# Optimization experiments

Hardware: AMD Instinct MI355X
Metric: run time of the kernel (lower is better)

The kernel has to match this reference:

```python
import jax, jax.numpy as jnp
import numpy as np

B, S, D_IN, D_OUT = 4, 4096, 256, 256

def setup_inputs() -> dict:
    key = jax.random.key(0)
    ks = jax.random.split(key, 7)
    scale = 1.0 / np.sqrt(D_IN)
    return {
        "x": jax.random.normal(ks[0], (B, S, D_IN), dtype=jnp.float32),
        "Wq": jax.random.uniform(ks[1], (D_IN, D_OUT), jnp.float32, -scale, scale),
        "bq": jax.random.uniform(ks[2], (D_OUT,), jnp.float32, -scale, scale),
        "Wk": jax.random.uniform(ks[3], (D_IN, D_OUT), jnp.float32, -scale, scale),
        "bk": jax.random.uniform(ks[4], (D_OUT,), jnp.float32, -scale, scale),
        "Wv": jax.random.uniform(ks[5], (D_IN, D_OUT), jnp.float32, -scale, scale),
        "bv": jax.random.uniform(ks[6], (D_OUT,), jnp.float32, -scale, scale),
    }

def reference(x, Wq, bq, Wk, bk, Wv, bv):
    # QKV projections: [B, S, D_OUT]
    q = jnp.einsum("bsd,de->bse", x, Wq) + bq
    k = jnp.einsum("bsd,de->bse", x, Wk) + bk
    v = jnp.einsum("bsd,de->bse", x, Wv) + bv
    # Scaled dot-product attention; full [B, S, S] scores as in the original.
    scores = jnp.einsum("bqe,bke->bqk", q, k) / jnp.sqrt(jnp.asarray(q.shape[-1], q.dtype))
    attn = jax.nn.softmax(scores, axis=-1)
    return jnp.einsum("bqk,bke->bqe", attn, v)
```

## Files before the change

kernel.cpp:

```cpp
#include <hip/hip_runtime.h>
#include <stdint.h>

typedef unsigned short u16;
typedef long long i64;
typedef __attribute__((ext_vector_type(4))) float f32x4;
typedef __attribute__((ext_vector_type(8))) short bf16x8;
typedef __attribute__((ext_vector_type(4))) int i32x4;
typedef __attribute__((ext_vector_type(2))) unsigned int u32x2;

#define SEQ 4096
#define DIM 256
#define QS4 0.36067376f

__device__ __forceinline__ u16 f2bf(float f) {
  union { float f; uint32_t u; } v; v.f = f;
  uint32_t r = (v.u + 0x7FFFu + ((v.u >> 16) & 1u)) >> 16;
  return (u16)r;
}

__device__ __forceinline__ uint8_t f2fp8(float f) {
  return (uint8_t)__builtin_amdgcn_cvt_pk_fp8_f32(f, 0.f, 0, false);
}

__device__ __forceinline__ void gload_lds16(const void* g, void* lds) {
  __builtin_amdgcn_global_load_lds(
      (const __attribute__((address_space(1))) uint32_t*)g,
      (__attribute__((address_space(3))) uint32_t*)lds, 16, 0, 0);
}

__device__ __forceinline__ f32x4 mfma8(i64 a, i64 b, f32x4 c) {
  return __builtin_amdgcn_mfma_f32_16x16x32_fp8_fp8(a, b, c, 0, 0, 0);
}

__global__ __launch_bounds__(256) void wt_kernel(const float* __restrict__ Wq,
                                                 const float* __restrict__ Wk,
                                                 const float* __restrict__ Wv,
                                                 u16* __restrict__ wt) {
  int b = blockIdx.x;
  int w = b >> 8;
  int n = b & 255;
  const float* W = (w == 0) ? Wq : ((w == 1) ? Wk : Wv);
  float scale = (w == 0) ? QS4 : ((w == 1) ? 0.25f : 1.0f);
  int k = threadIdx.x;
  wt[(w * 256 + n) * 256 + k] = f2bf(W[k * 256 + n] * scale);
}

__global__ __launch_bounds__(256) void qkv_kernel(
    const float* __restrict__ x, const float* __restrict__ bq,
    const float* __restrict__ bk, const float* __restrict__ bv,
    const u16* __restrict__ wt, uint8_t* __restrict__ qs,
    uint8_t* __restrict__ kk, char* __restrict__ vt) {
  __shared__ __align__(16) char lds_b[65536];
  __shared__ __align__(16) u16 lds_v[4096];
  int tid = threadIdx.x;
  int w = tid >> 6, l = tid & 63;
  int a = l & 15, g = l >> 4;
  int rowbase = blockIdx.x * 64;

  uint32_t wso[8];
#pragma unroll
  for (int j = 0; j < 8; ++j) {
    uint32_t inst = w * 8 + j;
    uint32_t flat = inst * 1024 + l * 16;
    uint32_t row = flat >> 9;
    uint32_t c5 = (flat >> 4) & 31;
    uint32_t sc = (c5 & ~7u) | ((c5 ^ row) & 7u);
    wso[j] = row * 512 + sc * 16;
  }
  uint32_t bro[8];
#pragma unroll
  for (int ks = 0; ks < 8; ++ks) {
    uint32_t c5 = ks * 4 + g;
    uint32_t sc = (c5 & ~7u) | ((c5 ^ (a & 7u)) & 7u);
    bro[ks] = (uint32_t)a * 512 + sc * 16;
  }

  bf16x8 afr[8];
  {
    int row = rowbase + w * 16 + a;
    const f32x4* xr4 = (const f32x4*)(x + (size_t)row * 256);
#pragma unroll
    for (int ks = 0; ks < 8; ++ks) {
      int q4 = ks * 8 + g * 2;
      f32x4 lo = xr4[q4], hi = xr4[q4 + 1];
      union { bf16x8 s; u16 u[8]; } fr;
      fr.u[0] = f2bf(lo[0]); fr.u[1] = f2bf(lo[1]);
      fr.u[2] = f2bf(lo[2]); fr.u[3] = f2bf(lo[3]);
      fr.u[4] = f2bf(hi[0]); fr.u[5] = f2bf(hi[1]);
      fr.u[6] = f2bf(hi[2]); fr.u[7] = f2bf(hi[3]);
      afr[ks] = fr.s;
    }
  }

#pragma unroll
  for (int j = 0; j < 8; ++j)
    gload_lds16((const char*)wt + wso[j], lds_b + (w * 8 + j) * 1024);

  int cur = 0;
  for (int it = 0; it < 12; ++it) {
    asm volatile("s_waitcnt vmcnt(0) lgkmcnt(0)" ::: "memory");
    __builtin_amdgcn_s_barrier();
    __builtin_amdgcn_sched_barrier(0);
    if (it < 11) {
#pragma unroll
      for (int j = 0; j < 8; ++j)
        gload_lds16((const char*)wt + (size_t)(it + 1) * 32768 + wso[j],
                    lds_b + (cur ^ 1) * 32768 + (w * 8 + j) * 1024);
    }
    int w3 = it >> 2, qn = it & 3;
    f32x4 acc[4];
#pragma unroll
    for (int n0 = 0; n0 < 4; ++n0) acc[n0] = (f32x4){0.f, 0.f, 0.f, 0.f};
#pragma unroll
    for (int ks = 0; ks < 8; ++ks) {
#pragma unroll
      for (int n0 = 0; n0 < 4; ++n0) {
        bf16x8 bfr = *(const bf16x8*)(lds_b + cur * 32768 + bro[ks] + n0 * 8192);
        acc[n0] = __builtin_amdgcn_mfma_f32_16x16x32_bf16(afr[ks], bfr, acc[n0], 0, 0, 0);
      }
    }
    const float* bias = (w3 == 0) ? bq : ((w3 == 1) ? bk : bv);
    if (w3 < 2) {
      uint8_t* out8 = (w3 == 0) ? qs : kk;
      float bscale = (w3 == 0) ? QS4 : 0.25f;
#pragma unroll
      for (int n0 = 0; n0 < 4; ++n0) {
        int col = qn * 64 + n0 * 16 + a;
        float bb = bias[col] * bscale;
#pragma unroll
        for (int r = 0; r < 4; ++r) {
          int row = rowbase + w * 16 + g * 4 + r;
          out8[(size_t)row * 256 + col] = f2fp8(acc[n0][r] + bb);
        }
      }
    } else {
#pragma unroll
      for (int n0 = 0; n0 < 4; ++n0) {
        int col = qn * 64 + n0 * 16 + a;
        float bb = bias[col];
        int dl = n0 * 16 + a;
#pragma unroll
        for (int r = 0; r < 4; ++r) {
          int m = w * 16 + g * 4 + r;
          uint32_t byteoff =
              (uint32_t)dl * 128 + ((((uint32_t)m >> 3) ^ ((uint32_t)dl & 7)) << 4) + (m & 7) * 2;
          *(u16*)((char*)lds_v + byteoff) = f2bf(acc[n0][r] + bb);
        }
      }
      asm volatile("s_waitcnt lgkmcnt(0)" ::: "memory");
      __builtin_amdgcn_s_barrier();
      {
        int dl = tid >> 2;
        size_t base = (size_t)blockIdx.x * 32768 + (size_t)(qn * 64 + dl) * 128;
#pragma unroll
        for (int cc = 0; cc < 2; ++cc) {
          uint32_t c = (tid & 3) + cc * 4;
          i32x4 vd = *(const i32x4*)((const char*)lds_v + dl * 128 + ((c ^ (dl & 7)) << 4));
          *(i32x4*)(vt + base + c * 16) = vd;
        }
      }
    }
    cur ^= 1;
  }
}

#define VVB 32768u
#define PVB 98304u

#define PV_STEP(SLOT)                                                          \
  {                                                                            \
    bf16x8 pfr[2][2];                                                          \
    _Pragma("unroll") for (int mt = 0; mt < 2; ++mt)                           \
    _Pragma("unroll") for (int j2 = 0; j2 < 2; ++j2)                           \
        pfr[mt][j2] = *(const bf16x8*)(lds + PVB + (SLOT) * 16384 + pro[j2] +  \
                                       mt * 2048);                             \
    __builtin_amdgcn_s_setprio(1);                                             \
    _Pragma("unroll") for (int mt = 0; mt < 2; ++mt)                           \
    _Pragma("unroll") for (int j2 = 0; j2 < 2; ++j2)                           \
        lacc[mt] = __builtin_amdgcn_mfma_f32_16x16x32_bf16(pfr[mt][j2], ones,  \
                                                           lacc[mt], 0, 0, 0); \
    _Pragma("unroll") for (int d0 = 0; d0 < 8; ++d0)                           \
    _Pragma("unroll") for (int j2 = 0; j2 < 2; ++j2) {                         \
      bf16x8 vfr = *(const bf16x8*)(lds + VVB + (SLOT) * 32768 + vro[j2] +     \
                                    d0 * 2048);                                \
      o[0][d0] = __builtin_amdgcn_mfma_f32_16x16x32_bf16(pfr[0][j2], vfr, o[0][d0], 0, 0, 0); \
      o[1][d0] = __builtin_amdgcn_mfma_f32_16x16x32_bf16(pfr[1][j2], vfr, o[1][d0], 0, 0, 0); \
    }                                                                          \
    __builtin_amdgcn_s_setprio(0);                                             \
  }

#define TILE(CUR, DO_PV, DO_K)                                                 \
  {                                                                            \
    asm volatile("s_waitcnt vmcnt(0) lgkmcnt(0)" ::: "memory");                \
    __builtin_amdgcn_s_barrier();                                              \
    __builtin_amdgcn_sched_barrier(0);                                         \
    _Pragma("unroll") for (int j = 0; j < 4; ++j)                              \
        gload_lds16(vstp + vso[j], lds + VVB + (CUR) * 32768 + (w * 4 + j) * 1024); \
    if (DO_K) {                                                                \
      gload_lds16(kstp + kso[0], lds + ((CUR) ^ 1) * 16384 + (w * 2 + 0) * 1024); \
      gload_lds16(kstp + kso[1], lds + ((CUR) ^ 1) * 16384 + (w * 2 + 1) * 1024); \
    }                                                                          \
    kstp += 16384;                                                             \
    vstp += 32768;                                                             \
    f32x4 sc[2][2];                                                            \
    _Pragma("unroll") for (int mt = 0; mt < 2; ++mt)                           \
    _Pragma("unroll") for (int n = 0; n < 2; ++n)                              \
        sc[mt][n] = (f32x4){0.f, 0.f, 0.f, 0.f};                               \
    __builtin_amdgcn_s_setprio(1);                                             \
    _Pragma("unroll") for (int n = 0; n < 2; ++n)                              \
    _Pragma("unroll") for (int j = 0; j < 8; ++j) {                            \
      i64 kfr = *(const i64*)(lds + (CUR) * 16384 + kro[j] + n * 4096);        \
      sc[0][n] = mfma8(kfr, qfr[0][j], sc[0][n]);                              \
      sc[1][n] = mfma8(kfr, qfr[1][j], sc[1][n]);                              \
    }                                                                          \
    __builtin_amdgcn_s_setprio(0);                                             \
    _Pragma("unroll") for (int mt = 0; mt < 2; ++mt)                           \
    _Pragma("unroll") for (int n = 0; n < 2; ++n) {                            \
      float e0 = exp2f(sc[mt][n][0]);                                          \
      float e1 = exp2f(sc[mt][n][1]);                                          \
      float e2 = exp2f(sc[mt][n][2]);                                          \
      float e3 = exp2f(sc[mt][n][3]);                                          \
      uint32_t p0 = (uint32_t)f2bf(e0) | ((uint32_t)f2bf(e1) << 16);           \
      uint32_t p1 = (uint32_t)f2bf(e2) | ((uint32_t)f2bf(e3) << 16);           \
      u32x2 pk = {p0, p1};                                                     \
      *(u32x2*)(lds + PVB + (CUR) * 16384 + pwo[n] + mt * 2048) = pk;          \
    }                                                                          \
    if (DO_PV) PV_STEP((CUR) ^ 1)                                              \
  }

__global__ __launch_bounds__(512, 1) void attn_kernel(
    const uint8_t* __restrict__ qs, const uint8_t* __restrict__ kk,
    const char* __restrict__ vt, float* __restrict__ out,
    float* __restrict__ pOB, float* __restrict__ pl, int split) {
  __shared__ __align__(16) char lds[131072];
  int tid = threadIdx.x;
  int w = tid >> 6, l = tid & 63;
  int a = l & 15, g = l >> 4;
  int qq = w >> 1, sub = w & 1;
  int bx = blockIdx.x;
  int h, batch, qt;
  if (split == 2) { h = bx & 1; batch = (bx >> 1) & 3; qt = bx >> 3; }
  else            { h = 0;      batch = (bx >> 1) & 3; qt = ((bx >> 3) << 1) | (bx & 1); }
  int ntHalf = (split == 2) ? 16 : 32;

  uint32_t a7 = a & 7;
  uint32_t kro[8], vro[2], pro[2], pwo[2], kso[2], vso[4];
  {
    uint32_t row = (uint32_t)(sub * 32 + a);
#pragma unroll
    for (int j = 0; j < 8; ++j) {
      uint32_t c4 = j * 2 + (g >> 1);
      kro[j] = row * 256 + (((c4 & ~7u) | ((c4 ^ a7) & 7u)) << 4) + (g & 1) * 8;
    }
  }
#pragma unroll
  for (int j2 = 0; j2 < 2; ++j2)
    vro[j2] = (uint32_t)(sub * 128 + a) * 128 +
              ((((uint32_t)(j2 * 4 + g)) ^ a7) << 4);
  {
    uint32_t q = (uint32_t)(qq * 32 + a);
#pragma unroll
    for (int j2 = 0; j2 < 2; ++j2)
      pro[j2] = q * 128 + ((((uint32_t)(j2 * 4 + g)) ^ a7) << 4);
#pragma unroll
    for (int n = 0; n < 2; ++n)
      pwo[n] = q * 128 +
               ((((uint32_t)(sub * 4 + n * 2 + (g >> 1))) ^ a7) << 4) + (g & 1) * 8;
  }
#pragma unroll
  for (int j = 0; j < 2; ++j) {
    uint32_t inst = w * 2 + j, flat = inst * 1024 + l * 16;
    uint32_t row = flat >> 8, c4 = (flat >> 4) & 15;
    kso[j] = row * 256 + (((c4 & ~7u) | ((c4 ^ (row & 7u)) & 7u)) << 4);
  }
#pragma unroll
  for (int j = 0; j < 4; ++j) {
    uint32_t inst = w * 4 + j, flat = inst * 1024 + l * 16;
    uint32_t row = flat >> 7, c3 = (flat >> 4) & 7;
    vso[j] = row * 128 + ((c3 ^ (row & 7)) << 4);
  }

  i64 qfr[2][8];
  {
    const uint8_t* qp = qs + (size_t)(batch * SEQ + qt * 128) * 256;
#pragma unroll
    for (int mt = 0; mt < 2; ++mt)
#pragma unroll
      for (int j = 0; j < 8; ++j)
        qfr[mt][j] = *(const i64*)(qp + (size_t)(qq * 32 + mt * 16 + a) * 256 +
                                   j * 32 + g * 8);
  }

  f32x4 o[2][8];
  f32x4 lacc[2];
#pragma unroll
  for (int mt = 0; mt < 2; ++mt) {
    lacc[mt] = (f32x4){0.f, 0.f, 0.f, 0.f};
#pragma unroll
    for (int d0 = 0; d0 < 8; ++d0) o[mt][d0] = (f32x4){0.f, 0.f, 0.f, 0.f};
  }
  const short ob = (short)0x3F80;
  bf16x8 ones = {ob, ob, ob, ob, ob, ob, ob, ob};

  const uint8_t* kstp = kk + (size_t)batch * SEQ * 256 + (size_t)h * 2048 * 256;
  const char* vstp = vt + (size_t)batch * 64 * 32768 + (size_t)h * 32 * 32768;

  gload_lds16(kstp + kso[0], lds + (w * 2 + 0) * 1024);
  gload_lds16(kstp + kso[1], lds + (w * 2 + 1) * 1024);
  kstp += 16384;

  TILE(0, false, true)
  for (int tp = 0; tp < ntHalf - 1; ++tp) {
    TILE(1, true, true)
    TILE(0, true, true)
  }
  TILE(1, true, false)

  asm volatile("s_waitcnt vmcnt(0) lgkmcnt(0)" ::: "memory");
  __builtin_amdgcn_s_barrier();
  __builtin_amdgcn_sched_barrier(0);
  PV_STEP(1)

  float* po = (h == 0) ? out : pOB;
  size_t obase = (size_t)(batch * SEQ + qt * 128 + qq * 32) * 256 + sub * 128;
#pragma unroll
  for (int mt = 0; mt < 2; ++mt)
#pragma unroll
    for (int r = 0; r < 4; ++r) {
#pragma unroll
      for (int d0 = 0; d0 < 8; ++d0)
        po[obase + (size_t)(mt * 16 + g * 4 + r) * 256 + d0 * 16 + a] = o[mt][d0][r];
    }
  if (a == 0 && sub == 0) {
#pragma unroll
    for (int mt = 0; mt < 2; ++mt)
#pragma unroll
      for (int r = 0; r < 4; ++r)
        pl[h * 16384 + (batch * 32 + qt) * 128 + qq * 32 + mt * 16 + g * 4 + r] =
            lacc[mt][r];
  }
}

__global__ __launch_bounds__(256) void combine_kernel(float* __restrict__ out,
                                                      const float* __restrict__ pOB,
                                                      const float* __restrict__ pl,
                                                      int split) {
  int b = blockIdx.x;
  int tid = threadIdx.x;
  int batch = b >> 12;
  int rem = b & 4095;
  int qt = rem >> 7, ql = rem & 127;
  size_t idx = (size_t)b * 256 + tid;
  int li = (batch * 32 + qt) * 128 + ql;
  float lA = pl[li];
  float v;
  if (split == 2) {
    float lB = pl[16384 + li];
    v = (out[idx] + pOB[idx]) / (lA + lB);
  } else {
    v = out[idx] / lA;
  }
  out[idx] = v;
}

extern "C" void kernel_launch(void* const* d_in, const int* in_sizes, int n_in,
                              void* d_out, int out_size, void* d_ws, size_t ws_size,
                              hipStream_t stream) {
  const float* x = (const float*)d_in[0];
  const float* Wq = (const float*)d_in[1];
  const float* bq = (const float*)d_in[2];
  const float* Wk = (const float*)d_in[3];
  const float* bk = (const float*)d_in[4];
  const float* Wv = (const float*)d_in[5];
  const float* bv = (const float*)d_in[6];
  char* ws = (char*)d_ws;
  u16* wt = (u16*)ws;
  uint8_t* qs = (uint8_t*)(ws + 0x60000);
  uint8_t* kk = (uint8_t*)(ws + 0x460000);
  char* vt = ws + 0x860000;
  float* pl = (float*)(ws + 0x1060000);
  float* pOB = (float*)(ws + 0x1080000);
  int split = (ws_size >= 0x2080000ull) ? 2 : 1;
  wt_kernel<<<dim3(768), dim3(256), 0, stream>>>(Wq, Wk, Wv, wt);
  qkv_kernel<<<dim3(256), dim3(256), 0, stream>>>(x, bq, bk, bv, wt, qs, kk, vt);
  attn_kernel<<<dim3(split * 128), dim3(512), 0, stream>>>(qs, kk, vt, (float*)d_out,
                                                           pOB, pl, split);
  combine_kernel<<<dim3(16384), dim3(256), 0, stream>>>((float*)d_out, pOB, pl, split);
}
```

Measured before the change: 118.3 us.

## Stagger QK/PV order across odd/even waves and store split partial output in bf16

New measurement: 120.8 us. +2.1%, slower.

```diff
diff --git a/kernel.cpp b/kernel.cpp
--- a/kernel.cpp
+++ b/kernel.cpp
@@ -16,6 +16,11 @@
   union { float f; uint32_t u; } v; v.f = f;
   uint32_t r = (v.u + 0x7FFFu + ((v.u >> 16) & 1u)) >> 16;
   return (u16)r;
+}
+
+__device__ __forceinline__ float bf2f(u16 u) {
+  union { uint32_t u; float f; } v; v.u = ((uint32_t)u) << 16;
+  return v.f;
 }
 
 __device__ __forceinline__ uint8_t f2fp8(float f) {
@@ -189,19 +194,8 @@
     __builtin_amdgcn_s_setprio(0);                                             \
   }
 
-#define TILE(CUR, DO_PV, DO_K)                                                 \
+#define QKEXP(CUR)                                                             \
   {                                                                            \
-    asm volatile("s_waitcnt vmcnt(0) lgkmcnt(0)" ::: "memory");                \
-    __builtin_amdgcn_s_barrier();                                              \
-    __builtin_amdgcn_sched_barrier(0);                                         \
-    _Pragma("unroll") for (int j = 0; j < 4; ++j)                              \
-        gload_lds16(vstp + vso[j], lds + VVB + (CUR) * 32768 + (w * 4 + j) * 1024); \
-    if (DO_K) {                                                                \
-      gload_lds16(kstp + kso[0], lds + ((CUR) ^ 1) * 16384 + (w * 2 + 0) * 1024); \
-      gload_lds16(kstp + kso[1], lds + ((CUR) ^ 1) * 16384 + (w * 2 + 1) * 1024); \
-    }                                                                          \
-    kstp += 16384;                                                             \
-    vstp += 32768;                                                             \
     f32x4 sc[2][2];                                                            \
     _Pragma("unroll") for (int mt = 0; mt < 2; ++mt)                           \
     _Pragma("unroll") for (int n = 0; n < 2; ++n)                              \
@@ -225,13 +219,34 @@
       u32x2 pk = {p0, p1};                                                     \
       *(u32x2*)(lds + PVB + (CUR) * 16384 + pwo[n] + mt * 2048) = pk;          \
     }                                                                          \
-    if (DO_PV) PV_STEP((CUR) ^ 1)                                              \
+  }
+
+#define TILE(CUR, DO_PV, DO_K)                                                 \
+  {                                                                            \
+    asm volatile("s_waitcnt vmcnt(0) lgkmcnt(0)" ::: "memory");                \
+    __builtin_amdgcn_s_barrier();                                              \
+    __builtin_amdgcn_sched_barrier(0);                                         \
+    _Pragma("unroll") for (int j = 0; j < 4; ++j)                              \
+        gload_lds16(vstp + vso[j], lds + VVB + (CUR) * 32768 + (w * 4 + j) * 1024); \
+    if (DO_K) {                                                                \
+      gload_lds16(kstp + kso[0], lds + ((CUR) ^ 1) * 16384 + (w * 2 + 0) * 1024); \
+      gload_lds16(kstp + kso[1], lds + ((CUR) ^ 1) * 16384 + (w * 2 + 1) * 1024); \
+    }                                                                          \
+    kstp += 16384;                                                             \
+    vstp += 32768;                                                             \
+    if (w & 1) {                                                               \
+      if (DO_PV) PV_STEP((CUR) ^ 1)                                            \
+      QKEXP(CUR)                                                               \
+    } else {                                                                   \
+      QKEXP(CUR)                                                               \
+      if (DO_PV) PV_STEP((CUR) ^ 1)                                            \
+    }                                                                          \
   }
 
 __global__ __launch_bounds__(512, 1) void attn_kernel(
     const uint8_t* __restrict__ qs, const uint8_t* __restrict__ kk,
     const char* __restrict__ vt, float* __restrict__ out,
-    float* __restrict__ pOB, float* __restrict__ pl, int split) {
+    u16* __restrict__ pOB, float* __restrict__ pl, int split) {
   __shared__ __align__(16) char lds[131072];
   int tid = threadIdx.x;
   int w = tid >> 6, l = tid & 63;
@@ -321,16 +336,27 @@
   __builtin_amdgcn_sched_barrier(0);
   PV_STEP(1)
 
-  float* po = (h == 0) ? out : pOB;
   size_t obase = (size_t)(batch * SEQ + qt * 128 + qq * 32) * 256 + sub * 128;
-#pragma unroll
-  for (int mt = 0; mt < 2; ++mt)
-#pragma unroll
-    for (int r = 0; r < 4; ++r) {
-#pragma unroll
-      for (int d0 = 0; d0 < 8; ++d0)
-        po[obase + (size_t)(mt * 16 + g * 4 + r) * 256 + d0 * 16 + a] = o[mt][d0][r];
-    }
+  if (h == 0) {
+#pragma unroll
+    for (int mt = 0; mt < 2; ++mt)
+#pragma unroll
+      for (int r = 0; r < 4; ++r) {
+#pragma unroll
+        for (int d0 = 0; d0 < 8; ++d0)
+          out[obase + (size_t)(mt * 16 + g * 4 + r) * 256 + d0 * 16 + a] = o[mt][d0][r];
+      }
+  } else {
+#pragma unroll
+    for (int mt = 0; mt < 2; ++mt)
+#pragma unroll
+      for (int r = 0; r < 4; ++r) {
+#pragma unroll
+        for (int d0 = 0; d0 < 8; ++d0)
+          pOB[obase + (size_t)(mt * 16 + g * 4 + r) * 256 + d0 * 16 + a] =
+              f2bf(o[mt][d0][r]);
+      }
+  }
   if (a == 0 && sub == 0) {
 #pragma unroll
     for (int mt = 0; mt < 2; ++mt)
@@ -342,7 +368,7 @@
 }
 
 __global__ __launch_bounds__(256) void combine_kernel(float* __restrict__ out,
-                                                      const float* __restrict__ pOB,
+                                                      const u16* __restrict__ pOB,
                                                       const float* __restrict__ pl,
                                                       int split) {
   int b = blockIdx.x;
@@ -356,7 +382,7 @@
   float v;
   if (split == 2) {
     float lB = pl[16384 + li];
-    v = (out[idx] + pOB[idx]) / (lA + lB);
+    v = (out[idx] + bf2f(pOB[idx])) / (lA + lB);
   } else {
     v = out[idx] / lA;
   }
@@ -379,8 +405,8 @@
   uint8_t* kk = (uint8_t*)(ws + 0x460000);
   char* vt = ws + 0x860000;
   float* pl = (float*)(ws + 0x1060000);
-  float* pOB = (float*)(ws + 0x1080000);
-  int split = (ws_size >= 0x2080000ull) ? 2 : 1;
+  u16* pOB = (u16*)(ws + 0x1080000);
+  int split = (ws_size >= 0x1880000ull) ? 2 : 1;
   wt_kernel<<<dim3(768), dim3(256), 0, stream>>>(Wq, Wk, Wv, wt);
   qkv_kernel<<<dim3(256), dim3(256), 0, stream>>>(x, bq, bk, bv, wt, qs, kk, vt);
   attn_kernel<<<dim3(split * 128), dim3(512), 0, stream>>>(qs, kk, vt, (float*)d_out,
```
